# Kernel tuning notes

Hardware: AMD Instinct MI355X
Metric: run time of the kernel (lower is better)

## Reference

```python
import jax, jax.numpy as jnp
import numpy as np

B, L, D = 8, 2048, 512


def setup_inputs() -> dict:
    key = jax.random.key(0)
    ks = jax.random.split(key, 6)
    s = 0.02
    return {
        "q": jax.random.normal(ks[0], (B, L, D), jnp.float32),
        "k": jax.random.normal(ks[1], (B, L, D), jnp.float32),
        "v": jax.random.normal(ks[2], (B, L, D), jnp.float32),
        "Wq": jax.random.normal(ks[3], (D, D), jnp.float32) * s,
        "bq": jnp.zeros((D,), jnp.float32),
        "Wk": jax.random.normal(ks[4], (D, D), jnp.float32) * s,
        "bk": jnp.zeros((D,), jnp.float32),
        "Wv": jax.random.normal(ks[5], (D, D), jnp.float32) * s,
        "bv": jnp.zeros((D,), jnp.float32),
    }


def reference(q, k, v, Wq, bq, Wk, bk, Wv, bv):
    # Linear projections (torch Linear: x @ W.T + b)
    qp = jnp.einsum("bld,ed->ble", q, Wq) + bq
    kp = jnp.einsum("bld,ed->ble", k, Wk) + bk
    vp = jnp.einsum("bld,ed->ble", v, Wv) + bv
    # attn[b, i, j] = qp[b, i] . kp[b, j]   (no 1/sqrt(d) scaling in source)
    attn = jnp.einsum("bqd,bkd->bqk", qp, kp)
    # Faithful to torch.nn.Softmax(dim=1): normalize over the QUERY axis.
    attn = jax.nn.softmax(attn, axis=1)
    out = jnp.einsum("bqk,bkd->bqd", attn, vp)
    return out
```

## Files before the change

### kernel.cpp

```cpp
#include <hip/hip_runtime.h>
#include <math.h>


#define TKK 32

typedef __attribute__((ext_vector_type(8))) short bf16x8;
typedef __attribute__((ext_vector_type(4))) float floatx4;

typedef __attribute__((address_space(3))) short lds_short;
typedef const __attribute__((address_space(1))) short glob_short;

__device__ __forceinline__ short f2bf(float x) {
    unsigned u = __float_as_uint(x);
    u += 0x7fff + ((u >> 16) & 1);
    return (short)(u >> 16);
}
__device__ __forceinline__ float bf2f(short s) {
    return __uint_as_float(((unsigned)(unsigned short)s) << 16);
}

__global__ __launch_bounds__(256) void prep(
    const float* __restrict__ q, const float* __restrict__ k,
    const float* __restrict__ v,
    const float* __restrict__ Wq, const float* __restrict__ Wk,
    const float* __restrict__ Wv,
    short* __restrict__ q_bf, short* __restrict__ k_bf, short* __restrict__ v_bf,
    short* __restrict__ Wq_bf, short* __restrict__ Wk_bf, short* __restrict__ Wv_bf,
    float* __restrict__ colsum)
{
    const int b = blockIdx.x;
    const float* in = nullptr;
    short* out = nullptr;
    long long i;
    if (b < 12288) {
        const int z = b >> 12;
        in  = (z == 0) ? q    : (z == 1) ? k    : v;
        out = (z == 0) ? q_bf : (z == 1) ? k_bf : v_bf;
        i = ((long long)(b & 4095) * 256 + threadIdx.x) * 8;
    } else if (b < 12672) {
        const int z = (b - 12288) >> 7;
        in  = (z == 0) ? Wq    : (z == 1) ? Wk    : Wv;
        out = (z == 0) ? Wq_bf : (z == 1) ? Wk_bf : Wv_bf;
        i = ((long long)((b - 12288) & 127) * 256 + threadIdx.x) * 8;
    } else {
        colsum[(b - 12672) * 256 + threadIdx.x] = 0.f;
        return;
    }
    float4 x = *(const float4*)(in + i);
    float4 y = *(const float4*)(in + i + 4);
    bf16x8 r;
    r[0] = f2bf(x.x); r[1] = f2bf(x.y); r[2] = f2bf(x.z); r[3] = f2bf(x.w);
    r[4] = f2bf(y.x); r[5] = f2bf(y.y); r[6] = f2bf(y.z); r[7] = f2bf(y.w);
    *(bf16x8*)(out + i) = r;
}

template<int TMp, int TNp, int WM, int WN, int HAS_BIAS, int OUT_BF16>
__device__ __forceinline__ void gemm_body(
    const short* __restrict__ A, const short* __restrict__ B,
    const float* __restrict__ bias, void* __restrict__ C,
    int N, int K, int m0, int n0)
{
    __shared__ short As[TMp * TKK];
    __shared__ short Bs[TNp * TKK];
    constexpr int MI = TMp / (16 * WM);
    constexpr int NJ = TNp / (16 * WN);
    const int t    = threadIdx.x;
    const int wave = t >> 6;
    const int lane = t & 63;
    const int wm = (wave / WN) * (TMp / WM);
    const int wn = (wave % WN) * (TNp / WN);
    const int sr = lane >> 2;
    const int sc = (lane & 3) * 8;

    floatx4 acc[MI][NJ];
    #pragma unroll
    for (int i = 0; i < MI; ++i)
        #pragma unroll
        for (int j = 0; j < NJ; ++j)
            acc[i][j] = (floatx4){0.f, 0.f, 0.f, 0.f};

    for (int k0 = 0; k0 < K; k0 += TKK) {
        #pragma unroll
        for (int c = wave; c < TMp / 16; c += 4)
            __builtin_amdgcn_global_load_lds(
                (glob_short*)(A + (long long)(m0 + c * 16 + sr) * K + k0 + sc),
                (lds_short*)(As + c * 512), 16, 0, 0);
        #pragma unroll
        for (int c = wave; c < TNp / 16; c += 4)
            __builtin_amdgcn_global_load_lds(
                (glob_short*)(B + (long long)(n0 + c * 16 + sr) * K + k0 + sc),
                (lds_short*)(Bs + c * 512), 16, 0, 0);
        __syncthreads();
        bf16x8 af[MI], bfr[NJ];
        #pragma unroll
        for (int i = 0; i < MI; ++i)
            af[i] = *(const bf16x8*)&As[(wm + i * 16 + (lane & 15)) * TKK + (lane >> 4) * 8];
        #pragma unroll
        for (int j = 0; j < NJ; ++j)
            bfr[j] = *(const bf16x8*)&Bs[(wn + j * 16 + (lane & 15)) * TKK + (lane >> 4) * 8];
        #pragma unroll
        for (int i = 0; i < MI; ++i)
            #pragma unroll
            for (int j = 0; j < NJ; ++j)
                acc[i][j] = __builtin_amdgcn_mfma_f32_16x16x32_bf16(af[i], bfr[j], acc[i][j], 0, 0, 0);
        __syncthreads();
    }

    #pragma unroll
    for (int i = 0; i < MI; ++i) {
        const int rbase = m0 + wm + i * 16 + (lane >> 4) * 4;
        #pragma unroll
        for (int j = 0; j < NJ; ++j) {
            const int col = n0 + wn + j * 16 + (lane & 15);
            const float bb = HAS_BIAS ? bias[col] : 0.f;
            #pragma unroll
            for (int r = 0; r < 4; ++r) {
                const long long off = (long long)(rbase + r) * N + col;
                const float vvv = acc[i][j][r] + bb;
                if (OUT_BF16) ((short*)C)[off] = f2bf(vvv);
                else          ((float*)C)[off] = vvv;
            }
        }
    }
}

__global__ __launch_bounds__(256) void proj_gemm(
    const short* __restrict__ x0, const short* __restrict__ x1, const short* __restrict__ x2,
    const short* __restrict__ w0, const short* __restrict__ w1, const short* __restrict__ w2,
    const float* __restrict__ b0, const float* __restrict__ b1, const float* __restrict__ b2,
    short* __restrict__ y0, short* __restrict__ y1, short* __restrict__ y2,
    int N, int K)
{
    const int z = blockIdx.z;
    const short* A    = (z == 0) ? x0 : (z == 1) ? x1 : x2;
    const short* B    = (z == 0) ? w0 : (z == 1) ? w1 : w2;
    const float* bias = (z == 0) ? b0 : (z == 1) ? b1 : b2;
    short*       C    = (z == 0) ? y0 : (z == 1) ? y1 : y2;
    gemm_body<128, 128, 2, 2, 1, 1>(A, B, bias, C, N, K,
                                    blockIdx.x * 128, blockIdx.y * 128);
}

__global__ __launch_bounds__(256) void pv_gemm(
    const short* __restrict__ Eg, const short* __restrict__ vpTg,
    float* __restrict__ outg, int N, int K,
    long long sA, long long sB, long long sC)
{
    __shared__ short As[2][128 * TKK];
    __shared__ short Bs[2][64 * TKK];
    const int bz = blockIdx.z;
    const short* A = Eg   + (long long)bz * sA;
    const short* B = vpTg + (long long)bz * sB;
    float*       C = outg + (long long)bz * sC;

    const int m0 = blockIdx.x * 128;
    const int n0 = blockIdx.y * 64;
    const int t    = threadIdx.x;
    const int wave = t >> 6;
    const int lane = t & 63;
    const int wm = (wave >> 1) * 64;
    const int wn = (wave & 1)  * 32;
    const int sr = lane >> 2;
    const int sc = (lane & 3) * 8;

    floatx4 acc[4][2];
    #pragma unroll
    for (int i = 0; i < 4; ++i)
        #pragma unroll
        for (int j = 0; j < 2; ++j)
            acc[i][j] = (floatx4){0.f, 0.f, 0.f, 0.f};

    for (int k0 = 0; k0 < K; k0 += 2 * TKK) {
        #pragma unroll
        for (int h = 0; h < 2; ++h) {
            const int kk = k0 + h * TKK;
            #pragma unroll
            for (int c = wave; c < 8; c += 4)
                __builtin_amdgcn_global_load_lds(
                    (glob_short*)(A + (long long)(m0 + c * 16 + sr) * K + kk + sc),
                    (lds_short*)(As[h] + c * 512), 16, 0, 0);
            __builtin_amdgcn_global_load_lds(
                (glob_short*)(B + (long long)(n0 + wave * 16 + sr) * K + kk + sc),
                (lds_short*)(Bs[h] + wave * 512), 16, 0, 0);
        }
        __syncthreads();
        #pragma unroll
        for (int h = 0; h < 2; ++h) {
            bf16x8 af[4], bfr[2];
            #pragma unroll
            for (int i = 0; i < 4; ++i)
                af[i] = *(const bf16x8*)&As[h][(wm + i * 16 + (lane & 15)) * TKK + (lane >> 4) * 8];
            #pragma unroll
            for (int j = 0; j < 2; ++j)
                bfr[j] = *(const bf16x8*)&Bs[h][(wn + j * 16 + (lane & 15)) * TKK + (lane >> 4) * 8];
            #pragma unroll
            for (int i = 0; i < 4; ++i)
                #pragma unroll
                for (int j = 0; j < 2; ++j)
                    acc[i][j] = __builtin_amdgcn_mfma_f32_16x16x32_bf16(af[i], bfr[j], acc[i][j], 0, 0, 0);
        }
        __syncthreads();
    }

    #pragma unroll
    for (int i = 0; i < 4; ++i) {
        const int rbase = m0 + wm + i * 16 + (lane >> 4) * 4;
        #pragma unroll
        for (int j = 0; j < 2; ++j) {
            const int col = n0 + wn + j * 16 + (lane & 15);
            #pragma unroll
            for (int r = 0; r < 4; ++r)
                C[(long long)(rbase + r) * N + col] = acc[i][j][r];
        }
    }
}

__global__ __launch_bounds__(256) void gemm_nt_exp_colsum(
    const short* __restrict__ A, const short* __restrict__ B,
    short* __restrict__ E, float* __restrict__ colsum,
    int N, int K, long long sA, long long sB, long long sE)
{
    __shared__ short As[128 * TKK];
    __shared__ short Bs[128 * TKK];
    __shared__ float wsum[4][64];
    const int bz = blockIdx.z;
    A += (long long)bz * sA;
    B += (long long)bz * sB;
    E += (long long)bz * sE;
    colsum += (long long)bz * N;

    const int m0 = blockIdx.x * 128;
    const int n0 = blockIdx.y * 128;
    const int t    = threadIdx.x;
    const int wave = t >> 6;
    const int lane = t & 63;
    const int wm = (wave >> 1) * 64;
    const int wn = (wave & 1)  * 64;
    const int sr = lane >> 2;
    const int sc = (lane & 3) * 8;

    floatx4 acc[4][4];
    #pragma unroll
    for (int i = 0; i < 4; ++i)
        #pragma unroll
        for (int j = 0; j < 4; ++j)
            acc[i][j] = (floatx4){0.f, 0.f, 0.f, 0.f};

    for (int k0 = 0; k0 < K; k0 += TKK) {
        #pragma unroll
        for (int it = 0; it < 2; ++it) {
            const int chunk = it * 4 + wave;
            const int r = chunk * 16 + sr;
            __builtin_amdgcn_global_load_lds(
                (glob_short*)(A + (long long)(m0 + r) * K + k0 + sc),
                (lds_short*)(As + chunk * 512), 16, 0, 0);
            __builtin_amdgcn_global_load_lds(
                (glob_short*)(B + (long long)(n0 + r) * K + k0 + sc),
                (lds_short*)(Bs + chunk * 512), 16, 0, 0);
        }
        __syncthreads();
        bf16x8 af[4], bfr[4];
        #pragma unroll
        for (int i = 0; i < 4; ++i)
            af[i] = *(const bf16x8*)&As[(wm + i * 16 + (lane & 15)) * TKK + (lane >> 4) * 8];
        #pragma unroll
        for (int j = 0; j < 4; ++j)
            bfr[j] = *(const bf16x8*)&Bs[(wn + j * 16 + (lane & 15)) * TKK + (lane >> 4) * 8];
        #pragma unroll
        for (int i = 0; i < 4; ++i)
            #pragma unroll
            for (int j = 0; j < 4; ++j)
                acc[i][j] = __builtin_amdgcn_mfma_f32_16x16x32_bf16(af[i], bfr[j], acc[i][j], 0, 0, 0);
        __syncthreads();
    }

    float csum[4] = {0.f, 0.f, 0.f, 0.f};
    #pragma unroll
    for (int i = 0; i < 4; ++i) {
        const int rbase = wm + i * 16 + (lane >> 4) * 4;
        #pragma unroll
        for (int j = 0; j < 4; ++j) {
            const int col = wn + j * 16 + (lane & 15);
            #pragma unroll
            for (int r = 0; r < 4; ++r) {
                const float e = __expf(acc[i][j][r]);
                E[(long long)(m0 + rbase + r) * N + (n0 + col)] = f2bf(e);
                csum[j] += e;
            }
        }
    }
    #pragma unroll
    for (int j = 0; j < 4; ++j) {
        csum[j] += __shfl_xor(csum[j], 16);
        csum[j] += __shfl_xor(csum[j], 32);
    }
    if (lane < 16) {
        #pragma unroll
        for (int j = 0; j < 4; ++j)
            wsum[wave][j * 16 + lane] = csum[j];
    }
    __syncthreads();
    if (t < 128) {
        const float s = (t < 64) ? (wsum[0][t] + wsum[2][t])
                                 : (wsum[1][t - 64] + wsum[3][t - 64]);
        atomicAdd(&colsum[n0 + t], s);
    }
}

__global__ __launch_bounds__(256) void transpose_scale_bf16(
    const short* __restrict__ in, const float* __restrict__ colsum,
    short* __restrict__ out, int R, int Cc)
{
    __shared__ short tile[32][33];
    const int b = blockIdx.z;
    in  += (long long)b * R * Cc;
    out += (long long)b * R * Cc;
    colsum += (long long)b * R;
    const int c0 = blockIdx.x * 32, r0 = blockIdx.y * 32;
    const int tx = threadIdx.x & 31, ty = threadIdx.x >> 5;
    #pragma unroll
    for (int rr = ty; rr < 32; rr += 8) {
        const float rs = 1.f / colsum[r0 + rr];
        tile[rr][tx] = f2bf(bf2f(in[(long long)(r0 + rr) * Cc + c0 + tx]) * rs);
    }
    __syncthreads();
    #pragma unroll
    for (int rr = ty; rr < 32; rr += 8)
        out[(long long)(c0 + rr) * R + r0 + tx] = tile[tx][rr];
}

extern "C" void kernel_launch(void* const* d_in, const int* in_sizes, int n_in,
                              void* d_out, int out_size, void* d_ws, size_t ws_size,
                              hipStream_t stream) {
    const float* q  = (const float*)d_in[0];
    const float* k  = (const float*)d_in[1];
    const float* v  = (const float*)d_in[2];
    const float* Wq = (const float*)d_in[3];
    const float* bq = (const float*)d_in[4];
    const float* Wk = (const float*)d_in[5];
    const float* bk = (const float*)d_in[6];
    const float* Wv = (const float*)d_in[7];
    const float* bv = (const float*)d_in[8];
    float* out = (float*)d_out;

    const int Bb = 8, L = 2048, D = 512;
    const long long BLD = (long long)Bb * L * D;
    const long long BLL = (long long)Bb * L * L;
    const long long DD  = (long long)D * D;

    short* base  = (short*)d_ws;
    short* q_bf  = base;
    short* k_bf  = q_bf  + BLD;
    short* v_bf  = k_bf  + BLD;
    short* qp_bf = v_bf  + BLD;
    short* kp_bf = qp_bf + BLD;
    short* vp_bf = kp_bf + BLD;
    short* vpT   = vp_bf + BLD;
    short* Wq_bf = vpT   + BLD;
    short* Wk_bf = Wq_bf + DD;
    short* Wv_bf = Wk_bf + DD;
    short* E_bf  = Wv_bf + DD;
    float* colsum = (float*)(E_bf + BLL);

    dim3 blk(256);

    prep<<<dim3(12736), blk, 0, stream>>>(q, k, v, Wq, Wk, Wv,
                                          q_bf, k_bf, v_bf,
                                          Wq_bf, Wk_bf, Wv_bf, colsum);

    dim3 gproj((Bb * L) / 128, D / 128, 3);
    proj_gemm<<<gproj, blk, 0, stream>>>(q_bf, k_bf, v_bf,
                                         Wq_bf, Wk_bf, Wv_bf,
                                         bq, bk, bv,
                                         qp_bf, kp_bf, vp_bf, D, D);

    dim3 gS(L / 128, L / 128, Bb);
    gemm_nt_exp_colsum<<<gS, blk, 0, stream>>>(qp_bf, kp_bf, E_bf, colsum,
                                               L, D,
                                               (long long)L * D, (long long)L * D,
                                               (long long)L * L);

    dim3 gT(D / 32, L / 32, Bb);
    transpose_scale_bf16<<<gT, blk, 0, stream>>>(vp_bf, colsum, vpT, L, D);

    dim3 gO(L / 128, D / 64, Bb);
    pv_gemm<<<gO, blk, 0, stream>>>(E_bf, vpT, out, D, L,
                                    (long long)L * L, (long long)D * L,
                                    (long long)L * D);
}
```

Measured before the change: 308.7 us.

## Fold log2(e) into Q projection, use raw exp2, and load two K-tiles per sync

The Q projection output is pre-scaled by log2(e), so the attention-score kernel can use the hardware v_exp_f32 (exp2) instruction directly instead of __expf, which adds its own multiply. Separately, the score GEMM now loads two K-slices into two LDS buffers before each barrier. That halves the number of __syncthreads per K loop at the cost of doubled LDS usage. Rounding q' to bf16 after scaling slightly changes numerics.

```diff
diff --git a/kernel.cpp b/kernel.cpp
--- a/kernel.cpp
+++ b/kernel.cpp
@@ -17,6 +17,11 @@
 }
 __device__ __forceinline__ float bf2f(short s) {
     return __uint_as_float(((unsigned)(unsigned short)s) << 16);
+}
+__device__ __forceinline__ float exp2_fast(float x) {
+    float r;
+    asm("v_exp_f32 %0, %1" : "=v"(r) : "v"(x));
+    return r;
 }
 
 __global__ __launch_bounds__(256) void prep(
@@ -58,7 +63,7 @@
 __device__ __forceinline__ void gemm_body(
     const short* __restrict__ A, const short* __restrict__ B,
     const float* __restrict__ bias, void* __restrict__ C,
-    int N, int K, int m0, int n0)
+    int N, int K, int m0, int n0, float escale)
 {
     __shared__ short As[TMp * TKK];
     __shared__ short Bs[TNp * TKK];
@@ -116,7 +121,7 @@
             #pragma unroll
             for (int r = 0; r < 4; ++r) {
                 const long long off = (long long)(rbase + r) * N + col;
-                const float vvv = acc[i][j][r] + bb;
+                const float vvv = (acc[i][j][r] + bb) * escale;
                 if (OUT_BF16) ((short*)C)[off] = f2bf(vvv);
                 else          ((float*)C)[off] = vvv;
             }
@@ -136,8 +141,9 @@
     const short* B    = (z == 0) ? w0 : (z == 1) ? w1 : w2;
     const float* bias = (z == 0) ? b0 : (z == 1) ? b1 : b2;
     short*       C    = (z == 0) ? y0 : (z == 1) ? y1 : y2;
+    const float esc   = (z == 0) ? 1.4426950408889634f : 1.0f;
     gemm_body<128, 128, 2, 2, 1, 1>(A, B, bias, C, N, K,
-                                    blockIdx.x * 128, blockIdx.y * 128);
+                                    blockIdx.x * 128, blockIdx.y * 128, esc);
 }
 
 __global__ __launch_bounds__(256) void pv_gemm(
@@ -219,8 +225,8 @@
     short* __restrict__ E, float* __restrict__ colsum,
     int N, int K, long long sA, long long sB, long long sE)
 {
-    __shared__ short As[128 * TKK];
-    __shared__ short Bs[128 * TKK];
+    __shared__ short As[2][128 * TKK];
+    __shared__ short Bs[2][128 * TKK];
     __shared__ float wsum[4][64];
     const int bz = blockIdx.z;
     A += (long long)bz * sA;
@@ -245,31 +251,38 @@
         for (int j = 0; j < 4; ++j)
             acc[i][j] = (floatx4){0.f, 0.f, 0.f, 0.f};
 
-    for (int k0 = 0; k0 < K; k0 += TKK) {
-        #pragma unroll
-        for (int it = 0; it < 2; ++it) {
-            const int chunk = it * 4 + wave;
-            const int r = chunk * 16 + sr;
-            __builtin_amdgcn_global_load_lds(
-                (glob_short*)(A + (long long)(m0 + r) * K + k0 + sc),
-                (lds_short*)(As + chunk * 512), 16, 0, 0);
-            __builtin_amdgcn_global_load_lds(
-                (glob_short*)(B + (long long)(n0 + r) * K + k0 + sc),
-                (lds_short*)(Bs + chunk * 512), 16, 0, 0);
-        }
-        __syncthreads();
-        bf16x8 af[4], bfr[4];
-        #pragma unroll
-        for (int i = 0; i < 4; ++i)
-            af[i] = *(const bf16x8*)&As[(wm + i * 16 + (lane & 15)) * TKK + (lane >> 4) * 8];
-        #pragma unroll
-        for (int j = 0; j < 4; ++j)
-            bfr[j] = *(const bf16x8*)&Bs[(wn + j * 16 + (lane & 15)) * TKK + (lane >> 4) * 8];
-        #pragma unroll
-        for (int i = 0; i < 4; ++i)
+    for (int k0 = 0; k0 < K; k0 += 2 * TKK) {
+        #pragma unroll
+        for (int h = 0; h < 2; ++h) {
+            const int kk = k0 + h * TKK;
+            #pragma unroll
+            for (int it = 0; it < 2; ++it) {
+                const int chunk = it * 4 + wave;
+                const int r = chunk * 16 + sr;
+                __builtin_amdgcn_global_load_lds(
+                    (glob_short*)(A + (long long)(m0 + r) * K + kk + sc),
+                    (lds_short*)(As[h] + chunk * 512), 16, 0, 0);
+                __builtin_amdgcn_global_load_lds(
+                    (glob_short*)(B + (long long)(n0 + r) * K + kk + sc),
+                    (lds_short*)(Bs[h] + chunk * 512), 16, 0, 0);
+            }
+        }
+        __syncthreads();
+        #pragma unroll
+        for (int h = 0; h < 2; ++h) {
+            bf16x8 af[4], bfr[4];
+            #pragma unroll
+            for (int i = 0; i < 4; ++i)
+                af[i] = *(const bf16x8*)&As[h][(wm + i * 16 + (lane & 15)) * TKK + (lane >> 4) * 8];
             #pragma unroll
             for (int j = 0; j < 4; ++j)
-                acc[i][j] = __builtin_amdgcn_mfma_f32_16x16x32_bf16(af[i], bfr[j], acc[i][j], 0, 0, 0);
+                bfr[j] = *(const bf16x8*)&Bs[h][(wn + j * 16 + (lane & 15)) * TKK + (lane >> 4) * 8];
+            #pragma unroll
+            for (int i = 0; i < 4; ++i)
+                #pragma unroll
+                for (int j = 0; j < 4; ++j)
+                    acc[i][j] = __builtin_amdgcn_mfma_f32_16x16x32_bf16(af[i], bfr[j], acc[i][j], 0, 0, 0);
+        }
         __syncthreads();
     }
 
@@ -282,7 +295,7 @@
             const int col = wn + j * 16 + (lane & 15);
             #pragma unroll
             for (int r = 0; r < 4; ++r) {
-                const float e = __expf(acc[i][j][r]);
+                const float e = exp2_fast(acc[i][j][r]);
                 E[(long long)(m0 + rbase + r) * N + (n0 + col)] = f2bf(e);
                 csum[j] += e;
             }
```

After: 305.0 us. About the same (-1.2%).
